# Kernel tuning notes

Measured on AMD Instinct MI355X. Metric: run time of the kernel, lower is better.

## Reference

```python
import jax, jax.numpy as jnp
import numpy as np

NUM_HEADS = 8
EPS = 1e-12  # torch F.normalize eps


def _conv1x1(x, W, b):
    # x: [B,C,H,W], W: [O,C], b: [O]
    return jnp.einsum('bchw,oc->bohw', x, W) + b[None, :, None, None]


def _mdta(x, wq, bq, wk, bk, wv, bv, temp):
    # Restormer-style channel attention (dropout = identity in eval).
    B, C, H, W = x.shape
    hd = C // NUM_HEADS

    def proj(Wm, bm):
        return _conv1x1(x, Wm, bm).reshape(B, NUM_HEADS, hd, H * W)

    q = proj(wq, bq)
    k = proj(wk, bk)
    v = proj(wv, bv)
    qn = q / jnp.maximum(jnp.linalg.norm(q, axis=-1, keepdims=True), EPS)
    kn = k / jnp.maximum(jnp.linalg.norm(k, axis=-1, keepdims=True), EPS)
    attn = jnp.einsum('bhcn,bhdn->bhcd', qn, kn) * temp  # temp: [heads,1,1]
    attn = jax.nn.softmax(attn, axis=-1)
    out = jnp.einsum('bhcd,bhdn->bhcn', attn, v) + v
    return out.reshape(B, C, H, W) + x


def setup_inputs() -> dict:
    key = jax.random.key(0)
    ks = jax.random.split(key, 10)
    B, C, H, W = 4, 64, 256, 256
    s = 1.0 / np.sqrt(C)
    f32 = jnp.float32
    return {
        'x': jax.random.normal(ks[0], (B, C, H, W), f32),
        'y': jax.random.normal(ks[1], (B, C, H, W), f32),
        'wq': jax.random.normal(ks[2], (C, C), f32) * s,
        'bq': jnp.zeros((C,), f32),
        'wk': jax.random.normal(ks[3], (C, C), f32) * s,
        'bk': jnp.zeros((C,), f32),
        'wv': jax.random.normal(ks[4], (C, C), f32) * s,
        'bv': jnp.zeros((C,), f32),
        'temp': jnp.ones((NUM_HEADS, 1, 1), f32),
        'w_ch': jax.random.normal(ks[5], (C, C), f32) * s,
        'b_ch': jnp.zeros((C,), f32),
        'w_y': jax.random.normal(ks[6], (C, C), f32) * s,
        'w_aw': jax.random.normal(ks[7], (1, C), f32) * s,
        'b_aw': jnp.zeros((1,), f32),
    }


def reference(x, y, wq, bq, wk, bk, wv, bv, temp, w_ch, b_ch, w_y, w_aw, b_aw):
    B, C, H, W = x.shape
    x_attn = _mdta(x, wq, bq, wk, bk, wv, bv, temp)
    y_attn = _mdta(y, wq, bq, wk, bk, wv, bv, temp)
    x_t = x_attn.transpose(0, 2, 3, 1)  # [B,H,W,C]
    y_t = y_attn.transpose(0, 2, 3, 1)
    # spatial gating: tanh(affine(x) + affine(y)) -> scalar logit per pixel
    xk = jnp.tanh(jnp.einsum('bhwc,oc->bhwo', x_t, w_ch) + b_ch
                  + jnp.einsum('bhwc,oc->bhwo', y_t, w_y))
    logits = (jnp.einsum('bhwo,ko->bhwk', xk, w_aw) + b_aw)[..., 0]  # [B,H,W]
    weight = jax.nn.softmax(logits.reshape(B, -1), axis=-1).reshape(B, 1, H, W)
    # result = x_1 * weight + x_1 (x_1 is the ORIGINAL input, permuted)
    result1 = x * (weight + 1.0)
    result2 = y * (weight + 1.0)
    return result1, result2
```

## Files before the change

kernel.cpp:

```cpp
#include <hip/hip_runtime.h>
#include <hip/hip_bf16.h>

typedef unsigned short ushortt;

#define BB 4
#define CC 64
#define NN 65536
#define HEADS 8

typedef __attribute__((ext_vector_type(8))) short bf16x8;
typedef __attribute__((ext_vector_type(4))) float f32x4;

#define OFF_PG   0UL
#define OFF_G    1343488UL
#define OFF_S    1376256UL
#define OFF_U    1376768UL
#define OFF_V    1409536UL
#define OFF_PS   1442304UL
#define OFF_CV2  1442816UL
#define OFF_P    1475072UL
#define OFF_L    1508096UL

__device__ __forceinline__ ushortt f2bf(float f) {
    union { float f; unsigned int i; } v; v.f = f;
    unsigned int x = v.i;
    unsigned int r = x + 0x7FFFu + ((x >> 16) & 1u);
    return (ushortt)(r >> 16);
}

__device__ __forceinline__ bf16x8 ld_cvt(const float* p) {
    const f32x4 a = *(const f32x4*)p;
    const f32x4 b = *(const f32x4*)(p + 4);
    bf16x8 r;
    r[0] = (short)f2bf(a[0]); r[1] = (short)f2bf(a[1]);
    r[2] = (short)f2bf(a[2]); r[3] = (short)f2bf(a[3]);
    r[4] = (short)f2bf(b[0]); r[5] = (short)f2bf(b[1]);
    r[6] = (short)f2bf(b[2]); r[7] = (short)f2bf(b[3]);
    return r;
}

__device__ __forceinline__ float fast_tanh(float t) {
    const float e = __expf(t + t);
    return 1.f - 2.f * __builtin_amdgcn_rcpf(e + 1.f);
}

#define MFMA(a,b,c) __builtin_amdgcn_mfma_f32_16x16x32_bf16(a,b,c,0,0,0)

__global__ __launch_bounds__(256) void k_gram(const float* __restrict__ x,
                                              const float* __restrict__ y,
                                              float* __restrict__ ws) {
    const int chunk = blockIdx.x;
    const int b = blockIdx.y, z = blockIdx.z;
    const float* X = (z ? y : x) + (size_t)b * CC * NN;
    const int tid = threadIdx.x;
    const int wid = tid >> 6, lane = tid & 63;
    const int lr = lane & 15, lk = lane >> 4;

    f32x4 accG[10];
    f32x4 accS[4];
#pragma unroll
    for (int t = 0; t < 10; ++t) accG[t] = (f32x4){0.f, 0.f, 0.f, 0.f};
#pragma unroll
    for (int g = 0; g < 4; ++g) accS[g] = (f32x4){0.f, 0.f, 0.f, 0.f};
    bf16x8 ones;
#pragma unroll
    for (int j = 0; j < 8; ++j) ones[j] = (short)0x3F80;

    const int p0 = chunk * 1024 + wid * 256;
    for (int ks = 0; ks < 8; ++ks) {
        const int pc = p0 + ks * 32 + lk * 8;
        bf16x8 a0 = ld_cvt(X + (size_t)(0 * 16 + lr) * NN + pc);
        bf16x8 a1 = ld_cvt(X + (size_t)(1 * 16 + lr) * NN + pc);
        bf16x8 a2 = ld_cvt(X + (size_t)(2 * 16 + lr) * NN + pc);
        bf16x8 a3 = ld_cvt(X + (size_t)(3 * 16 + lr) * NN + pc);
        accG[0] = MFMA(a0, a0, accG[0]);
        accG[1] = MFMA(a0, a1, accG[1]);
        accG[2] = MFMA(a0, a2, accG[2]);
        accG[3] = MFMA(a0, a3, accG[3]);
        accG[4] = MFMA(a1, a1, accG[4]);
        accG[5] = MFMA(a1, a2, accG[5]);
        accG[6] = MFMA(a1, a3, accG[6]);
        accG[7] = MFMA(a2, a2, accG[7]);
        accG[8] = MFMA(a2, a3, accG[8]);
        accG[9] = MFMA(a3, a3, accG[9]);
        accS[0] = MFMA(a0, ones, accS[0]);
        accS[1] = MFMA(a1, ones, accS[1]);
        accS[2] = MFMA(a2, ones, accS[2]);
        accS[3] = MFMA(a3, ones, accS[3]);
    }

    __shared__ float red[2624];
    for (int i = tid; i < 2624; i += 256) red[i] = 0.f;
    __syncthreads();
    for (int w = 0; w < 4; ++w) {
        if (wid == w) {
#pragma unroll
            for (int ti = 0; ti < 4; ++ti)
#pragma unroll
                for (int tj = ti; tj < 4; ++tj) {
                    const int t = ti * 4 - ti * (ti + 1) / 2 + tj;
#pragma unroll
                    for (int r = 0; r < 4; ++r)
                        red[t * 256 + (lk * 4 + r) * 16 + lr] += accG[t][r];
                }
            if (lr == 0) {
#pragma unroll
                for (int g = 0; g < 4; ++g)
#pragma unroll
                    for (int r = 0; r < 4; ++r)
                        red[2560 + g * 16 + lk * 4 + r] += accS[g][r];
            }
        }
        __syncthreads();
    }
    const int slot = (z * 4 + b) * 64 + chunk;
    float* outp = ws + OFF_PG + (size_t)slot * 2624;
    for (int i = tid; i < 2624; i += 256) outp[i] = red[i];
}

__global__ void k_reduce(float* __restrict__ ws) {
    const int gid = blockIdx.x * 256 + threadIdx.x;
    if (gid < 8 * 4096) {
        const int zb = gid >> 12;
        const int e = gid & 4095;
        const int row = e >> 6, col = e & 63;
        const int ti = row >> 4, tj = col >> 4;
        int t, elem;
        if (ti <= tj) { t = ti * 4 - ti * (ti + 1) / 2 + tj; elem = (row & 15) * 16 + (col & 15); }
        else          { t = tj * 4 - tj * (tj + 1) / 2 + ti; elem = (col & 15) * 16 + (row & 15); }
        const float* base = ws + OFF_PG + (size_t)(zb * 64) * 2624 + t * 256 + elem;
        float s = 0.f;
        for (int c = 0; c < 64; ++c) s += base[(size_t)c * 2624];
        ws[OFF_G + gid] = s;
    } else if (gid < 8 * 4096 + 8 * 64) {
        const int g2 = gid - 8 * 4096;
        const int zb = g2 >> 6, e = g2 & 63;
        const float* base = ws + OFF_PG + (size_t)(zb * 64) * 2624 + 2560 + e;
        float s = 0.f;
        for (int c = 0; c < 64; ++c) s += base[(size_t)c * 2624];
        ws[OFF_S + g2] = s;
    }
}

__global__ void k_uv(const float* __restrict__ wq, const float* __restrict__ wk,
                     float* __restrict__ ws) {
    const int gid = blockIdx.x * 256 + threadIdx.x;
    const int which = gid >> 15;
    const int rem = gid & 32767;
    const int zb = rem >> 12;
    const int e = rem & 4095;
    const int r = e >> 6, j = e & 63;
    const float* W = which ? wk : wq;
    const float* Gm = ws + OFF_G + (size_t)zb * 4096;
    float acc = 0.f;
    for (int i = 0; i < 64; ++i) acc += W[r * 64 + i] * Gm[i * 64 + j];
    ws[(which ? OFF_V : OFF_U) + (size_t)zb * 4096 + e] = acc;
}

__global__ __launch_bounds__(256) void k_attn2(
        const float* __restrict__ wq, const float* __restrict__ bq,
        const float* __restrict__ wk, const float* __restrict__ bk,
        const float* __restrict__ wv, const float* __restrict__ bv,
        const float* __restrict__ temp,
        const float* __restrict__ w_ch, const float* __restrict__ b_ch,
        const float* __restrict__ w_y, float* __restrict__ ws) {
    const int zb = blockIdx.x;
    const int z = zb >> 2;
    const int tid = threadIdx.x;

    __shared__ float Ul[4096], Vl[4096];
    __shared__ float wql[4096], wkl[4096], wvl[4096], wsl[4096];
    __shared__ float sl[64], dq[64], dk[64], wqs[64], wks[64];
    __shared__ float qkl[512], Al[512], cstz[64];
    __shared__ float ph1s[64][4][4];

    {
        const float* Ug = ws + OFF_U + (size_t)zb * 4096;
        const float* Vg = ws + OFF_V + (size_t)zb * 4096;
        const float* wsel = z ? w_y : w_ch;
        for (int i = tid * 4; i < 4096; i += 1024) {
            *(f32x4*)(Ul + i)  = *(const f32x4*)(Ug + i);
            *(f32x4*)(Vl + i)  = *(const f32x4*)(Vg + i);
            *(f32x4*)(wql + i) = *(const f32x4*)(wq + i);
            *(f32x4*)(wkl + i) = *(const f32x4*)(wk + i);
            *(f32x4*)(wvl + i) = *(const f32x4*)(wv + i);
            *(f32x4*)(wsl + i) = *(const f32x4*)(wsel + i);
        }
        if (tid < 64) sl[tid] = ws[OFF_S + (size_t)zb * 64 + tid];
    }
    __syncthreads();

    {
        const int r = tid >> 2, q = tid & 3;
        float swq = 0.f, swk = 0.f, sqq = 0.f, skk = 0.f;
#pragma unroll
        for (int jj = 0; jj < 16; ++jj) {
            const int j = q * 16 + jj;
            const float svj = sl[j];
            const float wqv = wql[r * 64 + j];
            const float wkv = wkl[r * 64 + j];
            swq += wqv * svj; swk += wkv * svj;
            sqq += Ul[r * 64 + j] * wqv;
            skk += Vl[r * 64 + j] * wkv;
        }
        ph1s[r][q][0] = swq; ph1s[r][q][1] = swk;
        ph1s[r][q][2] = sqq; ph1s[r][q][3] = skk;
    }
    __syncthreads();
    if (tid < 64) {
        const int r = tid;
        const float swq = ph1s[r][0][0] + ph1s[r][1][0] + ph1s[r][2][0] + ph1s[r][3][0];
        const float swk = ph1s[r][0][1] + ph1s[r][1][1] + ph1s[r][2][1] + ph1s[r][3][1];
        float sqq = ph1s[r][0][2] + ph1s[r][1][2] + ph1s[r][2][2] + ph1s[r][3][2];
        float skk = ph1s[r][0][3] + ph1s[r][1][3] + ph1s[r][2][3] + ph1s[r][3][3];
        const float bqv = bq[r], bkv = bk[r];
        sqq += 2.f * bqv * swq + 65536.f * bqv * bqv;
        skk += 2.f * bkv * swk + 65536.f * bkv * bkv;
        dq[r] = fmaxf(sqrtf(fmaxf(sqq, 0.f)), 1e-12f);
        dk[r] = fmaxf(sqrtf(fmaxf(skk, 0.f)), 1e-12f);
        wqs[r] = swq; wks[r] = swk;
    }
    __syncthreads();
    for (int kq = 0; kq < 2; ++kq) {
        const int id = tid + kq * 256;
        const int h = id >> 6, o = (id >> 3) & 7, p = id & 7;
        const int r = h * 8 + o, c = h * 8 + p;
        float acc = 0.f;
#pragma unroll 8
        for (int j = 0; j < 64; ++j) acc += Ul[r * 64 + j] * wkl[c * 64 + j];
        const float bqv = bq[r], bkv = bk[c];
        acc += bqv * wks[c] + bkv * wqs[r] + 65536.f * bqv * bkv;
        qkl[id] = acc;
    }
    __syncthreads();
    if (tid < 64) {
        const int r = tid, h = r >> 3;
        const float tv = temp[h];
        float L[8];
        float m = -1e30f;
#pragma unroll
        for (int p = 0; p < 8; ++p) {
            const float v = qkl[h * 64 + (r & 7) * 8 + p] / (dq[r] * dk[h * 8 + p]) * tv;
            L[p] = v; m = fmaxf(m, v);
        }
        float s = 0.f;
#pragma unroll
        for (int p = 0; p < 8; ++p) { L[p] = __expf(L[p] - m); s += L[p]; }
        const float inv = 1.f / s;
        float cz = bv[r];
#pragma unroll
        for (int p = 0; p < 8; ++p) {
            const float a = L[p] * inv;
            Al[r * 8 + p] = a;
            cz += a * bv[h * 8 + p];
        }
        cstz[r] = cz;
    }
    __syncthreads();
    for (int o4 = tid; o4 < 4096; o4 += 256) {
        const int o = o4 >> 6, j = o4 & 63, hj = j >> 3;
        float m = 0.f;
#pragma unroll
        for (int p = 0; p < 8; ++p)
            m += wsl[o * 64 + hj * 8 + p] * Al[(hj * 8 + p) * 8 + (j & 7)];
        Vl[o4] = wsl[o4] + m;
    }
    __syncthreads();
    for (int o4 = tid; o4 < 4096; o4 += 256) {
        const int o = o4 >> 6, c = o4 & 63;
        float acc = wsl[o4];
#pragma unroll 8
        for (int j = 0; j < 64; ++j) acc += Vl[o * 64 + j] * wvl[j * 64 + c];
        ws[OFF_P + (size_t)zb * 4096 + o4] = acc;
    }
    if (tid < 64) {
        const int o = tid;
        float acc = z ? 0.f : b_ch[o];
        for (int r = 0; r < 64; ++r) acc += wsl[o * 64 + r] * cstz[r];
        ws[OFF_CV2 + (size_t)zb * 64 + o] = acc;
    }
}

#define LITER 8
__global__ __launch_bounds__(256, 2) void k_logits(const float* __restrict__ x,
        const float* __restrict__ y, const float* __restrict__ w_aw,
        const float* __restrict__ b_aw, float* __restrict__ ws) {
    const int b = blockIdx.y;
    const int bx = blockIdx.x;
    const int tid = threadIdx.x;
    const int wid = tid >> 6, lane = tid & 63;
    const int lr = lane & 15, lg = lane >> 4;

    const float* Pbase = ws + OFF_P + (size_t)b * 4096;
    const float* Qbase = ws + OFF_P + (size_t)(4 + b) * 4096;

    bf16x8 AP[4][2], AQ[4][2];
#pragma unroll
    for (int ot = 0; ot < 4; ++ot)
#pragma unroll
        for (int ks = 0; ks < 2; ++ks) {
            const int off = (ot * 16 + lr) * 64 + ks * 32 + lg * 8;
            AP[ot][ks] = ld_cvt(Pbase + off);
            AQ[ot][ks] = ld_cvt(Qbase + off);
        }

    float awr[4][4], cvr[4][4];
#pragma unroll
    for (int ot = 0; ot < 4; ++ot)
#pragma unroll
        for (int r = 0; r < 4; ++r) {
            const int o = ot * 16 + lg * 4 + r;
            awr[ot][r] = w_aw[o];
            cvr[ot][r] = ws[OFF_CV2 + b * 64 + o] + ws[OFF_CV2 + (4 + b) * 64 + o];
        }
    const float baw0 = b_aw[0];

    const float* xb = x + (size_t)b * CC * NN;
    const float* yb = y + (size_t)b * CC * NN;

    float esum = 0.f;
#pragma unroll 1
    for (int it = 0; it < LITER; ++it) {
        const int px0 = bx * (LITER * 64) + wid * (LITER * 16) + it * 16;
        bf16x8 BX[2], BY[2];
#pragma unroll
        for (int ks = 0; ks < 2; ++ks) {
            bf16x8 fx, fy;
#pragma unroll
            for (int j = 0; j < 8; ++j) {
                const size_t off = (size_t)(ks * 32 + lg * 8 + j) * NN + px0 + lr;
                fx[j] = (short)f2bf(xb[off]);
                fy[j] = (short)f2bf(yb[off]);
            }
            BX[ks] = fx; BY[ks] = fy;
        }
        f32x4 Cf[4];
#pragma unroll
        for (int ot = 0; ot < 4; ++ot) Cf[ot] = (f32x4){0.f, 0.f, 0.f, 0.f};
#pragma unroll
        for (int ot = 0; ot < 4; ++ot)
#pragma unroll
            for (int ks = 0; ks < 2; ++ks) {
                Cf[ot] = MFMA(AP[ot][ks], BX[ks], Cf[ot]);
                Cf[ot] = MFMA(AQ[ot][ks], BY[ks], Cf[ot]);
            }
        float partial = 0.f;
#pragma unroll
        for (int ot = 0; ot < 4; ++ot)
#pragma unroll
            for (int r = 0; r < 4; ++r)
                partial += awr[ot][r] * fast_tanh(Cf[ot][r] + cvr[ot][r]);
        partial += __shfl_xor(partial, 16);
        partial += __shfl_xor(partial, 32);
        const float e = __expf(partial + baw0);
        if (lane < 16)
            ws[OFF_L + (size_t)b * NN + px0 + lane] = e;
        esum += e * 0.25f;
    }
#pragma unroll
    for (int d = 1; d < 64; d <<= 1) esum += __shfl_xor(esum, d);
    __shared__ float wsum[4];
    if (lane == 0) wsum[wid] = esum;
    __syncthreads();
    if (tid == 0)
        ws[OFF_PS + (size_t)b * 128 + bx] = wsum[0] + wsum[1] + wsum[2] + wsum[3];
}

__global__ __launch_bounds__(256) void k_final(const float* __restrict__ x,
        const float* __restrict__ y, const float* __restrict__ ws,
        float* __restrict__ out) {
    const int gid = blockIdx.x * 256 + threadIdx.x;
    const int b = gid >> 19;
    const int lane = threadIdx.x & 63;
    float s = ws[OFF_PS + (size_t)b * 128 + lane] + ws[OFF_PS + (size_t)b * 128 + 64 + lane];
#pragma unroll
    for (int d = 1; d < 64; d <<= 1) s += __shfl_xor(s, d);
    const float inv = 1.f / s;

    const int rem = gid & 524287;
    const int c = rem >> 13;
    const int n0 = (rem & 8191) * 8;
    const float* w = ws + OFF_L + (size_t)b * NN + n0;
    const f32x4 w0 = *(const f32x4*)w;
    const f32x4 w1 = *(const f32x4*)(w + 4);
    const size_t idx = ((size_t)(b * 64 + c)) * NN + n0;
    const f32x4 x0 = *(const f32x4*)(x + idx);
    const f32x4 x1 = *(const f32x4*)(x + idx + 4);
    const f32x4 y0 = *(const f32x4*)(y + idx);
    const f32x4 y1 = *(const f32x4*)(y + idx + 4);
    f32x4 o0, o1, o2, o3;
#pragma unroll
    for (int j = 0; j < 4; ++j) {
        const float s0 = 1.f + w0[j] * inv;
        const float s1 = 1.f + w1[j] * inv;
        o0[j] = x0[j] * s0;
        o1[j] = x1[j] * s1;
        o2[j] = y0[j] * s0;
        o3[j] = y1[j] * s1;
    }
    *(f32x4*)(out + idx) = o0;
    *(f32x4*)(out + idx + 4) = o1;
    *(f32x4*)(out + 16777216UL + idx) = o2;
    *(f32x4*)(out + 16777216UL + idx + 4) = o3;
}

extern "C" void kernel_launch(void* const* d_in, const int* in_sizes, int n_in,
                              void* d_out, int out_size, void* d_ws, size_t ws_size,
                              hipStream_t stream) {
    const float* x    = (const float*)d_in[0];
    const float* y    = (const float*)d_in[1];
    const float* wq   = (const float*)d_in[2];
    const float* bq   = (const float*)d_in[3];
    const float* wk   = (const float*)d_in[4];
    const float* bk   = (const float*)d_in[5];
    const float* wv   = (const float*)d_in[6];
    const float* bv   = (const float*)d_in[7];
    const float* temp = (const float*)d_in[8];
    const float* wch  = (const float*)d_in[9];
    const float* bch  = (const float*)d_in[10];
    const float* wyy  = (const float*)d_in[11];
    const float* waw  = (const float*)d_in[12];
    const float* baw  = (const float*)d_in[13];
    float* out = (float*)d_out;
    float* ws = (float*)d_ws;

    hipLaunchKernelGGL(k_gram, dim3(64, 4, 2), dim3(256), 0, stream, x, y, ws);
    hipLaunchKernelGGL(k_reduce, dim3(130), dim3(256), 0, stream, ws);
    hipLaunchKernelGGL(k_uv, dim3(256), dim3(256), 0, stream, wq, wk, ws);
    hipLaunchKernelGGL(k_attn2, dim3(8), dim3(256), 0, stream,
                       wq, bq, wk, bk, wv, bv, temp, wch, bch, wyy, ws);
    hipLaunchKernelGGL(k_logits, dim3(128, 4), dim3(256), 0, stream, x, y, waw, baw, ws);
    hipLaunchKernelGGL(k_final, dim3(8192), dim3(256), 0, stream, x, y, ws, out);
}
```

Before: 136.7 us.

## Fuse U/V projection into attention kernel and retile logits with hoisted loads

Removes the separate k_uv kernel and computes U=Wq·G and V=Wk·G inside the attention kernel from the Gram matrix staged in shared memory. This saves a launch and a global round trip, but makes the 8-block kernel do more serial work. The logits kernel halves pixels per block (grid doubles to 256x4), fully unrolls the loop, and issues all 32 x/y loads before the bf16 conversion to raise memory-level parallelism. k_final now reads 256 partial sums per batch and reduces them once per block through shared memory.

```diff
diff --git a/kernel.cpp b/kernel.cpp
--- a/kernel.cpp
+++ b/kernel.cpp
@@ -14,10 +14,8 @@
 #define OFF_PG   0UL
 #define OFF_G    1343488UL
 #define OFF_S    1376256UL
-#define OFF_U    1376768UL
-#define OFF_V    1409536UL
 #define OFF_PS   1442304UL
-#define OFF_CV2  1442816UL
+#define OFF_CV2  1443328UL
 #define OFF_P    1475072UL
 #define OFF_L    1508096UL
 
@@ -142,22 +140,7 @@
     }
 }
 
-__global__ void k_uv(const float* __restrict__ wq, const float* __restrict__ wk,
-                     float* __restrict__ ws) {
-    const int gid = blockIdx.x * 256 + threadIdx.x;
-    const int which = gid >> 15;
-    const int rem = gid & 32767;
-    const int zb = rem >> 12;
-    const int e = rem & 4095;
-    const int r = e >> 6, j = e & 63;
-    const float* W = which ? wk : wq;
-    const float* Gm = ws + OFF_G + (size_t)zb * 4096;
-    float acc = 0.f;
-    for (int i = 0; i < 64; ++i) acc += W[r * 64 + i] * Gm[i * 64 + j];
-    ws[(which ? OFF_V : OFF_U) + (size_t)zb * 4096 + e] = acc;
-}
-
-__global__ __launch_bounds__(256) void k_attn2(
+__global__ __launch_bounds__(256) void k_attn3(
         const float* __restrict__ wq, const float* __restrict__ bq,
         const float* __restrict__ wk, const float* __restrict__ bk,
         const float* __restrict__ wv, const float* __restrict__ bv,
@@ -168,25 +151,36 @@
     const int z = zb >> 2;
     const int tid = threadIdx.x;
 
-    __shared__ float Ul[4096], Vl[4096];
+    __shared__ float Gl[4096], Ul[4096], Vl[4096];
     __shared__ float wql[4096], wkl[4096], wvl[4096], wsl[4096];
     __shared__ float sl[64], dq[64], dk[64], wqs[64], wks[64];
     __shared__ float qkl[512], Al[512], cstz[64];
     __shared__ float ph1s[64][4][4];
 
     {
-        const float* Ug = ws + OFF_U + (size_t)zb * 4096;
-        const float* Vg = ws + OFF_V + (size_t)zb * 4096;
+        const float* Gg = ws + OFF_G + (size_t)zb * 4096;
         const float* wsel = z ? w_y : w_ch;
         for (int i = tid * 4; i < 4096; i += 1024) {
-            *(f32x4*)(Ul + i)  = *(const f32x4*)(Ug + i);
-            *(f32x4*)(Vl + i)  = *(const f32x4*)(Vg + i);
+            *(f32x4*)(Gl + i)  = *(const f32x4*)(Gg + i);
             *(f32x4*)(wql + i) = *(const f32x4*)(wq + i);
             *(f32x4*)(wkl + i) = *(const f32x4*)(wk + i);
             *(f32x4*)(wvl + i) = *(const f32x4*)(wv + i);
             *(f32x4*)(wsl + i) = *(const f32x4*)(wsel + i);
         }
         if (tid < 64) sl[tid] = ws[OFF_S + (size_t)zb * 64 + tid];
+    }
+    __syncthreads();
+
+    for (int o4 = tid; o4 < 4096; o4 += 256) {
+        const int r = o4 >> 6, j = o4 & 63;
+        float au = 0.f, av = 0.f;
+#pragma unroll 8
+        for (int i = 0; i < 64; ++i) {
+            const float g = Gl[i * 64 + j];
+            au += wql[r * 64 + i] * g;
+            av += wkl[r * 64 + i] * g;
+        }
+        Ul[o4] = au; Vl[o4] = av;
     }
     __syncthreads();
 
@@ -281,7 +275,7 @@
     }
 }
 
-#define LITER 8
+#define LITER 4
 __global__ __launch_bounds__(256, 2) void k_logits(const float* __restrict__ x,
         const float* __restrict__ y, const float* __restrict__ w_aw,
         const float* __restrict__ b_aw, float* __restrict__ ws) {
@@ -315,22 +309,31 @@
         }
     const float baw0 = b_aw[0];
 
-    const float* xb = x + (size_t)b * CC * NN;
-    const float* yb = y + (size_t)b * CC * NN;
+    const float* xb = x + (size_t)b * CC * NN + bx * (LITER * 16) * 4 ;
+    const int pxw = bx * 256 + wid * 64;
+    const float* xw = x + (size_t)b * CC * NN + pxw;
+    const float* yw = y + (size_t)b * CC * NN + pxw;
+    (void)xb;
 
     float esum = 0.f;
-#pragma unroll 1
+#pragma unroll
     for (int it = 0; it < LITER; ++it) {
-        const int px0 = bx * (LITER * 64) + wid * (LITER * 16) + it * 16;
+        const int px = it * 16 + lr;
+        float fxr[16], fyr[16];
+#pragma unroll
+        for (int j = 0; j < 16; ++j) {
+            const size_t off = (size_t)((j >> 3) * 32 + lg * 8 + (j & 7)) * NN + px;
+            fxr[j] = xw[off];
+            fyr[j] = yw[off];
+        }
         bf16x8 BX[2], BY[2];
 #pragma unroll
         for (int ks = 0; ks < 2; ++ks) {
             bf16x8 fx, fy;
 #pragma unroll
             for (int j = 0; j < 8; ++j) {
-                const size_t off = (size_t)(ks * 32 + lg * 8 + j) * NN + px0 + lr;
-                fx[j] = (short)f2bf(xb[off]);
-                fy[j] = (short)f2bf(yb[off]);
+                fx[j] = (short)f2bf(fxr[ks * 8 + j]);
+                fy[j] = (short)f2bf(fyr[ks * 8 + j]);
             }
             BX[ks] = fx; BY[ks] = fy;
         }
@@ -354,7 +357,7 @@
         partial += __shfl_xor(partial, 32);
         const float e = __expf(partial + baw0);
         if (lane < 16)
-            ws[OFF_L + (size_t)b * NN + px0 + lane] = e;
+            ws[OFF_L + (size_t)b * NN + pxw + it * 16 + lane] = e;
         esum += e * 0.25f;
     }
 #pragma unroll
@@ -363,7 +366,7 @@
     if (lane == 0) wsum[wid] = esum;
     __syncthreads();
     if (tid == 0)
-        ws[OFF_PS + (size_t)b * 128 + bx] = wsum[0] + wsum[1] + wsum[2] + wsum[3];
+        ws[OFF_PS + (size_t)b * 256 + bx] = wsum[0] + wsum[1] + wsum[2] + wsum[3];
 }
 
 __global__ __launch_bounds__(256) void k_final(const float* __restrict__ x,
@@ -371,11 +374,18 @@
         float* __restrict__ out) {
     const int gid = blockIdx.x * 256 + threadIdx.x;
     const int b = gid >> 19;
-    const int lane = threadIdx.x & 63;
-    float s = ws[OFF_PS + (size_t)b * 128 + lane] + ws[OFF_PS + (size_t)b * 128 + 64 + lane];
-#pragma unroll
-    for (int d = 1; d < 64; d <<= 1) s += __shfl_xor(s, d);
-    const float inv = 1.f / s;
+    const int tid = threadIdx.x;
+
+    __shared__ float invs;
+    if (tid < 64) {
+        const float* ps = ws + OFF_PS + (size_t)b * 256;
+        float s = ps[tid] + ps[64 + tid] + ps[128 + tid] + ps[192 + tid];
+#pragma unroll
+        for (int d = 1; d < 64; d <<= 1) s += __shfl_xor(s, d);
+        if (tid == 0) invs = 1.f / s;
+    }
+    __syncthreads();
+    const float inv = invs;
 
     const int rem = gid & 524287;
     const int c = rem >> 13;
@@ -426,9 +436,8 @@
 
     hipLaunchKernelGGL(k_gram, dim3(64, 4, 2), dim3(256), 0, stream, x, y, ws);
     hipLaunchKernelGGL(k_reduce, dim3(130), dim3(256), 0, stream, ws);
-    hipLaunchKernelGGL(k_uv, dim3(256), dim3(256), 0, stream, wq, wk, ws);
-    hipLaunchKernelGGL(k_attn2, dim3(8), dim3(256), 0, stream,
+    hipLaunchKernelGGL(k_attn3, dim3(8), dim3(256), 0, stream,
                        wq, bq, wk, bk, wv, bv, temp, wch, bch, wyy, ws);
-    hipLaunchKernelGGL(k_logits, dim3(128, 4), dim3(256), 0, stream, x, y, waw, baw, ws);
+    hipLaunchKernelGGL(k_logits, dim3(256, 4), dim3(256), 0, stream, x, y, waw, baw, ws);
     hipLaunchKernelGGL(k_final, dim3(8192), dim3(256), 0, stream, x, y, ws, out);
 }
```

Measured after the change: 151.9 us. +11.1%, slower.
